# Kernel optimization log

Measured on AMD Instinct MI355X. Metric: run time of the kernel, lower is better.

## Reference

```python
import jax, jax.numpy as jnp
import numpy as np

P = 8  # patch size
EPS = 1e-5

def ln_ch(x, w, b):
    # WithBias LayerNorm over channel dim of (B,C,H,W): torch code flattens to (B,HW,C) and norms last dim
    mu = x.mean(axis=1, keepdims=True)
    var = ((x - mu) ** 2).mean(axis=1, keepdims=True)
    return (x - mu) / jnp.sqrt(var + EPS) * w[None, :, None, None] + b[None, :, None, None]

def conv1x1(x, w):
    # w: [C_out, C_in]
    return jnp.einsum('bchw,oc->bohw', x, w)

def dwconv3x3(x, w):
    # depthwise 3x3, w: [C,1,3,3]
    return jax.lax.conv_general_dilated(x, w, (1, 1), 'SAME', dimension_numbers=('NCHW', 'OIHW', 'NCHW'), feature_group_count=x.shape[1])

def patchify(x):
    b, c, H, W = x.shape
    return x.reshape(b, c, H // P, P, W // P, P).transpose(0, 1, 2, 4, 3, 5)  # b c h w p1 p2

def unpatchify(x):
    b, c, h, w, p1, p2 = x.shape
    return x.transpose(0, 1, 2, 4, 3, 5).reshape(b, c, h * p1, w * p2)

def setup_inputs() -> dict:
    key = jax.random.key(0)
    ks = jax.random.split(key, 16)
    B, C, H, W = 4, 64, 256, 256
    hid = 2 * C  # ffn_expansion_factor=2
    s = 0.02
    return {
        'x': jax.random.normal(ks[0], (B, C, H, W), jnp.float32),
        'evt': jax.random.normal(ks[1], (B, C, H, W), jnp.float32),
        'ln1i_w': jnp.ones((C,), jnp.float32), 'ln1i_b': jnp.zeros((C,), jnp.float32),
        'ln1e_w': jnp.ones((C,), jnp.float32), 'ln1e_b': jnp.zeros((C,), jnp.float32),
        'w_q': jax.random.normal(ks[2], (2 * C, C), jnp.float32) * s,
        'dw_q': jax.random.normal(ks[3], (2 * C, 1, 3, 3), jnp.float32) * s,
        'w_kv': jax.random.normal(ks[4], (4 * C, C), jnp.float32) * s,
        'dw_kv': jax.random.normal(ks[5], (4 * C, 1, 3, 3), jnp.float32) * s,
        'lnA_w': jnp.ones((2 * C,), jnp.float32), 'lnA_b': jnp.zeros((2 * C,), jnp.float32),
        'w_po_attn': jax.random.normal(ks[6], (C, 2 * C), jnp.float32) * s,
        'ln2_w': jnp.ones((C,), jnp.float32), 'ln2_b': jnp.zeros((C,), jnp.float32),
        'w_pi': jax.random.normal(ks[7], (2 * hid, C), jnp.float32) * s,
        'fft_param': jnp.ones((2 * hid, 1, 1, P, P // 2 + 1), jnp.float32),
        'dw_ffn': jax.random.normal(ks[8], (2 * hid, 1, 3, 3), jnp.float32) * s,
        'w_po_ffn': jax.random.normal(ks[9], (C, hid), jnp.float32) * s,
    }

def reference(x, evt, ln1i_w, ln1i_b, ln1e_w, ln1e_b, w_q, dw_q, w_kv, dw_kv, lnA_w, lnA_b, w_po_attn, ln2_w, ln2_b, w_pi, fft_param, dw_ffn, w_po_ffn):
    # ---- EventFSAS cross attention ----
    xn = ln_ch(x, ln1i_w, ln1i_b)
    en = ln_ch(evt, ln1e_w, ln1e_b)
    q = dwconv3x3(conv1x1(xn, w_q), dw_q)               # (B,2C,H,W)
    kv = dwconv3x3(conv1x1(en, w_kv), dw_kv)            # (B,4C,H,W)
    k, v = jnp.split(kv, 2, axis=1)
    qf = jnp.fft.rfft2(patchify(q))                      # (B,2C,h,w,8,5) complex
    kf = jnp.fft.rfft2(patchify(k))
    out = jnp.fft.irfft2(qf * kf, s=(P, P))
    out = ln_ch(unpatchify(out), lnA_w, lnA_b)
    x = x + conv1x1(v * out, w_po_attn)
    # ---- DFFN ----
    y = conv1x1(ln_ch(x, ln2_w, ln2_b), w_pi)            # (B,4C,H,W)
    yf = jnp.fft.rfft2(patchify(y)) * fft_param
    y = unpatchify(jnp.fft.irfft2(yf, s=(P, P)))
    y = dwconv3x3(y, dw_ffn)
    y1, y2 = jnp.split(y, 2, axis=1)
    y = jax.nn.gelu(y1, approximate=False) * y2          # torch nn.GELU is exact erf form
    return x + conv1x1(y, w_po_ffn)
```

## Files before the change

### kernel.cpp

```cpp
#include <hip/hip_runtime.h>

#define HW 65536
#define NPOS 262144

typedef unsigned int   u32;
typedef unsigned short u16;
typedef __attribute__((ext_vector_type(8))) short v8s;
typedef __attribute__((ext_vector_type(4))) float f32x4;
typedef __attribute__((ext_vector_type(2))) float f32x2;

__device__ __forceinline__ float bf2f(u16 h){
  union { u32 u; float f; } c; c.u = ((u32)h) << 16; return c.f;
}
__device__ __forceinline__ u16 f2bf(float f){
  union { u32 u; float f; } c; c.f = f;
  u32 r = c.u + 0x7fffu + ((c.u >> 16) & 1u);
  return (u16)(r >> 16);
}
__device__ __forceinline__ u32 pk2(float a, float b){
  return (u32)f2bf(a) | ((u32)f2bf(b) << 16);
}
__device__ __forceinline__ v8s as8(uint4 u){
  union { uint4 a; v8s b; } c; c.a = u; return c.b;
}
__device__ __forceinline__ f32x2 up2(u32 u){
  union { u32 u; float f; } lo, hi;
  lo.u = u << 16; hi.u = u & 0xffff0000u;
  f32x2 r; r.x = lo.f; r.y = hi.f; return r;
}
__device__ __forceinline__ float gelu_exact(float x){
  return 0.5f*x*(1.0f+erff(x*0.70710678118654752f));
}

__device__ void fold_w(const float* __restrict__ W, int rows,
                       const float* __restrict__ lw, const float* __restrict__ lb,
                       u16* __restrict__ Wf, float* __restrict__ A, float* __restrict__ B){
  int tid = threadIdx.x;
  for (int e = tid; e < rows*64; e += 256) Wf[e] = f2bf(lw[e & 63] * W[e]);
  for (int r = tid; r < rows; r += 256){
    float a = 0.f, b2 = 0.f;
    for (int c = 0; c < 64; c++){ float w = W[r*64+c]; a += lw[c]*w; b2 += lb[c]*w; }
    A[r] = a; B[r] = b2;
  }
}

__global__ void k_prep(const float* __restrict__ M, float* __restrict__ g,
    const float* wq,  const float* l1iw, const float* l1ib, u16* wqf,  float* aq,  float* bq,
    const float* wkv, const float* l1ew, const float* l1eb, u16* wkvf, float* akv, float* bkv,
    const float* wpi, const float* l2w,  const float* l2b,  u16* wpif, float* api, float* bpi,
    const float* wpa, u16* wpaf, const float* wpf, u16* wpff)
{
  int blk = blockIdx.x, tid = threadIdx.x;
  if (blk < 64){
    int t = blk*256 + tid;
    int c = t >> 6, uv = t & 63, u = uv >> 3, v = uv & 7;
    const float* mc = M + c*40;
    const float ctab[8] = {1.f, 0.70710678118654752f, 0.f, -0.70710678118654752f,
                           -1.f, -0.70710678118654752f, 0.f, 0.70710678118654752f};
    float acc = 0.f;
    for (int k1=0;k1<8;k1++)
      for (int k2=0;k2<8;k2++){
        float s = (k2<=4) ? mc[k1*5+k2] : mc[(((8-k1)&7)*5) + (8-k2)];
        acc += s * ctab[(k1*u + k2*v)&7];
      }
    g[t] = acc * (1.f/64.f);
  } else if (blk == 64){ fold_w(wq, 128, l1iw, l1ib, wqf, aq, bq); }
  else if (blk == 65){ fold_w(wkv, 256, l1ew, l1eb, wkvf, akv, bkv); }
  else if (blk == 66){ fold_w(wpi, 256, l2w, l2b, wpif, api, bpi); }
  else if (blk == 67){ for (int e=tid; e<64*128; e+=256) wpaf[e] = f2bf(wpa[e]); }
  else               { for (int e=tid; e<64*128; e+=256) wpff[e] = f2bf(wpf[e]); }
}

__global__ void k_prep2(const float* __restrict__ g, u16* __restrict__ CM){
  int c = blockIdx.x;
  const float* gc = g + (size_t)c*64;
  u16* cm = CM + (size_t)c*4096;
  for (int e = threadIdx.x; e < 4096; e += 256){
    int o = e >> 6, i = e & 63;
    int du = ((o>>3) - (i>>3)) & 7, dv = ((o&7) - (i&7)) & 7;
    cm[e] = f2bf(gc[du*8 + dv]);
  }
}

struct GA {
  const float* src; const u16* Wf; const float* Af; const float* Bf;
  u32* dst; int o0; int dstOffP; int Cdp; int b0; int pxbase;
};

template<int NZ>
__global__ __launch_bounds__(256) void k_gemm64(GA a0, GA a1){
  GA a = (blockIdx.y == 0) ? a0 : a1;
  __shared__ uint4 lsX[128*8];
  __shared__ uint4 lsW[64*NZ*8];
  __shared__ float2 sPart[256];
  __shared__ float2 sStat[128];
  int tid = threadIdx.x;
  int px = tid & 127, hf = tid >> 7;
  int p0 = a.pxbase + blockIdx.x*128;
  int b = p0 >> 16, hwb = p0 & 65535;
  {
    const uint4* wsrc = (const uint4*)(a.Wf + (size_t)a.o0*64);
    #pragma unroll
    for (int i=0; i<NZ*2; i++){
      int idx = i*256 + tid, row = idx>>3, s = idx&7;
      lsW[row*8 + (s ^ (row&7))] = wsrc[idx];
    }
  }
  {
    const float* sp = a.src + (size_t)b*64*HW + hwb + px + (size_t)(hf*32)*HW;
    float e[32];
    #pragma unroll
    for (int c=0;c<32;c++) e[c] = sp[(size_t)c*HW];
    float sm = 0.f, sq = 0.f;
    #pragma unroll
    for (int c=0;c<32;c++){ sm += e[c]; sq += e[c]*e[c]; }
    uint4* xrow = lsX + px*8;
    #pragma unroll
    for (int sl=0; sl<4; sl++){
      uint4 pkv;
      pkv.x = pk2(e[sl*8+0], e[sl*8+1]); pkv.y = pk2(e[sl*8+2], e[sl*8+3]);
      pkv.z = pk2(e[sl*8+4], e[sl*8+5]); pkv.w = pk2(e[sl*8+6], e[sl*8+7]);
      xrow[(hf*4+sl) ^ (px&7)] = pkv;
    }
    sPart[tid] = make_float2(sm, sq);
  }
  __syncthreads();
  if (tid < 128){
    float2 A = sPart[tid], B = sPart[tid+128];
    float s = A.x + B.x, q = A.y + B.y;
    float mu = s*(1.f/64.f);
    float var = q*(1.f/64.f) - mu*mu;
    sStat[tid] = make_float2(mu, rsqrtf(fmaxf(var,0.f)+1e-5f));
  }
  __syncthreads();
  int w = tid>>6, l = tid&63, g = l>>4, c15 = l&15;
  float2 stv[2];
  #pragma unroll
  for (int pp=0;pp<2;pp++) stv[pp] = sStat[w*32 + pp*16 + c15];

  #pragma unroll
  for (int z=0; z<NZ; z++){
    f32x4 acc[2][4];
    #pragma unroll
    for (int pp=0;pp<2;pp++)
      #pragma unroll
      for (int po=0;po<4;po++) acc[pp][po] = (f32x4){0.f,0.f,0.f,0.f};
    #pragma unroll
    for (int kk=0; kk<2; kk++){
      v8s wf[4], xf[2];
      #pragma unroll
      for (int po=0;po<4;po++){ int row = z*64 + po*16 + c15; wf[po] = as8(lsW[row*8 + ((kk*4+g) ^ (row&7))]); }
      #pragma unroll
      for (int pp=0;pp<2;pp++){ int row = w*32 + pp*16 + c15; xf[pp] = as8(lsX[row*8 + ((kk*4+g) ^ (row&7))]); }
      #pragma unroll
      for (int pp=0;pp<2;pp++)
        #pragma unroll
        for (int po=0;po<4;po++)
          acc[pp][po] = __builtin_amdgcn_mfma_f32_16x16x32_bf16(wf[po], xf[pp], acc[pp][po], 0,0,0);
    }
    size_t obaseP = ((size_t)(b - a.b0)*a.Cdp + a.dstOffP + z*32)*HW + hwb + w*32;
    #pragma unroll
    for (int po=0;po<4;po++)
      #pragma unroll
      for (int j2=0;j2<2;j2++){
        int oc = po*16 + g*4 + j2*2;
        float A0 = a.Af[a.o0 + z*64 + oc],   B0 = a.Bf[a.o0 + z*64 + oc];
        float A1 = a.Af[a.o0 + z*64 + oc+1], B1 = a.Bf[a.o0 + z*64 + oc+1];
        int ocp = po*8 + g*2 + j2;
        u32* dp = a.dst + obaseP + (size_t)ocp*HW + c15;
        #pragma unroll
        for (int pp=0;pp<2;pp++){
          float lo = stv[pp].y*(acc[pp][po][j2*2  ] - stv[pp].x*A0) + B0;
          float hi = stv[pp].y*(acc[pp][po][j2*2+1] - stv[pp].x*A1) + B1;
          dp[pp*16] = pk2(lo, hi);
        }
      }
  }
}

__global__ __launch_bounds__(256) void k_gemm_attn(
    const float* __restrict__ x, const u32* __restrict__ orawp, const u32* __restrict__ vbp,
    const float* __restrict__ lnw, const float* __restrict__ lnb,
    const u16* __restrict__ Wf, float* __restrict__ out)
{
  __shared__ uint4 lsX[128*16];
  __shared__ uint4 lsW[64*16];
  __shared__ float2 sPart[256];
  __shared__ float2 sStat[128];
  int tid = threadIdx.x;
  int p0 = blockIdx.x*128;
  int b = p0 >> 16, hwb = p0 & 65535;
  int px = tid & 127, hf = tid >> 7;
  {
    const uint4* wsrc = (const uint4*)Wf;
    #pragma unroll
    for (int i=0;i<4;i++){
      int idx = i*256 + tid, row = idx>>4, s = idx&15;
      lsW[row*16 + (s ^ (row&15))] = wsrc[idx];
    }
  }
  const u32* orp = orawp + ((size_t)b*64 + hf*32)*HW + hwb + px;
  {
    u32 r32[32];
    #pragma unroll
    for (int i=0;i<32;i++) r32[i] = orp[(size_t)i*HW];
    float sum = 0.f, ssq = 0.f;
    #pragma unroll
    for (int sl=0; sl<8; sl++){
      u32 wds[4];
      #pragma unroll
      for (int q2=0;q2<4;q2++){
        u32 wv = r32[sl*4+q2];
        float fl = bf2f((u16)(wv&0xffff)), fh = bf2f((u16)(wv>>16));
        sum += fl + fh; ssq += fl*fl + fh*fh;
        wds[q2] = wv;
      }
      int s = hf*8 + sl;
      lsX[px*16 + (s ^ (px&15))] = make_uint4(wds[0],wds[1],wds[2],wds[3]);
    }
    sPart[tid] = make_float2(sum, ssq);
  }
  __syncthreads();
  if (tid < 128){
    float2 A = sPart[tid], B = sPart[tid+128];
    float s = A.x + B.x, q = A.y + B.y;
    float mu = s*(1.f/128.f);
    float var = q*(1.f/128.f) - mu*mu;
    sStat[tid] = make_float2(mu, rsqrtf(fmaxf(var,0.f)+1e-5f));
  }
  __syncthreads();
  {
    float2 st = sStat[px];
    const u32* vp = vbp + ((size_t)b*64 + hf*32)*HW + hwb + px;
    u32 v32[32];
    #pragma unroll
    for (int i=0;i<32;i++) v32[i] = vp[(size_t)i*HW];
    #pragma unroll
    for (int sl=0; sl<8; sl++){
      int s = hf*8 + sl;
      int li = px*16 + (s ^ (px&15));
      uint4 raw = lsX[li];
      u32 wds[4] = {raw.x, raw.y, raw.z, raw.w};
      u32 ow[4];
      #pragma unroll
      for (int q2=0;q2<4;q2++){
        int ch = hf*64 + sl*8 + q2*2;
        float e0 = bf2f((u16)(wds[q2]&0xffff)), e1 = bf2f((u16)(wds[q2]>>16));
        u32 vv = v32[sl*4+q2];
        float v0 = bf2f((u16)(vv&0xffff)), v1 = bf2f((u16)(vv>>16));
        float r0 = ((e0-st.x)*st.y*lnw[ch  ] + lnb[ch  ])*v0;
        float r1 = ((e1-st.x)*st.y*lnw[ch+1] + lnb[ch+1])*v1;
        ow[q2] = pk2(r0, r1);
      }
      lsX[li] = make_uint4(ow[0],ow[1],ow[2],ow[3]);
    }
  }
  __syncthreads();
  int w4 = tid>>6, l = tid&63, g = l>>4, c15 = l&15;
  f32x4 acc[2][4];
  #pragma unroll
  for (int pp=0;pp<2;pp++)
    #pragma unroll
    for (int po=0;po<4;po++) acc[pp][po] = (f32x4){0.f,0.f,0.f,0.f};
  #pragma unroll
  for (int kk=0; kk<4; kk++){
    v8s wf[4], xf[2];
    #pragma unroll
    for (int po=0;po<4;po++){ int row = po*16 + c15; wf[po] = as8(lsW[row*16 + ((kk*4+g) ^ (row&15))]); }
    #pragma unroll
    for (int pp=0;pp<2;pp++){ int row = w4*32 + pp*16 + c15; xf[pp] = as8(lsX[row*16 + ((kk*4+g) ^ (row&15))]); }
    #pragma unroll
    for (int pp=0;pp<2;pp++)
      #pragma unroll
      for (int po=0;po<4;po++)
        acc[pp][po] = __builtin_amdgcn_mfma_f32_16x16x32_bf16(wf[po], xf[pp], acc[pp][po], 0,0,0);
  }
  size_t obase = (size_t)b*64*HW + hwb + w4*32;
  #pragma unroll
  for (int po=0;po<4;po++)
    #pragma unroll
    for (int j=0;j<4;j++){
      int oc = po*16 + g*4 + j;
      const float* xs = x + obase + (size_t)oc*HW + c15;
      float* dp = out + obase + (size_t)oc*HW + c15;
      #pragma unroll
      for (int pp=0;pp<2;pp++) dp[pp*16] = xs[pp*16] + acc[pp][po][j];
    }
}

__global__ __launch_bounds__(256) void k_gemm_ffn(
    const u32* __restrict__ y3gp, const u16* __restrict__ Wf, float* __restrict__ out,
    int pxbase, int b0)
{
  __shared__ uint4 lsX[128*16];
  __shared__ uint4 lsW[64*16];
  int tid = threadIdx.x;
  int p0 = pxbase + blockIdx.x*128;
  int b = p0 >> 16, hwb = p0 & 65535;
  int px = tid & 127, hf = tid >> 7;
  {
    const uint4* wsrc = (const uint4*)Wf;
    #pragma unroll
    for (int i=0;i<4;i++){
      int idx = i*256 + tid, row = idx>>4, s = idx&15;
      lsW[row*16 + (s ^ (row&15))] = wsrc[idx];
    }
  }
  const u32* yp = y3gp + ((size_t)(b-b0)*64 + hf*32)*HW + hwb + px;
  {
    u32 r32[32];
    #pragma unroll
    for (int i=0;i<32;i++) r32[i] = yp[(size_t)i*HW];
    #pragma unroll
    for (int sl=0; sl<8; sl++){
      int s = hf*8 + sl;
      lsX[px*16 + (s ^ (px&15))] = make_uint4(r32[sl*4+0],r32[sl*4+1],r32[sl*4+2],r32[sl*4+3]);
    }
  }
  __syncthreads();
  int w4 = tid>>6, l = tid&63, g = l>>4, c15 = l&15;
  f32x4 acc[2][4];
  #pragma unroll
  for (int pp=0;pp<2;pp++)
    #pragma unroll
    for (int po=0;po<4;po++) acc[pp][po] = (f32x4){0.f,0.f,0.f,0.f};
  #pragma unroll
  for (int kk=0; kk<4; kk++){
    v8s wf[4], xf[2];
    #pragma unroll
    for (int po=0;po<4;po++){ int row = po*16 + c15; wf[po] = as8(lsW[row*16 + ((kk*4+g) ^ (row&15))]); }
    #pragma unroll
    for (int pp=0;pp<2;pp++){ int row = w4*32 + pp*16 + c15; xf[pp] = as8(lsX[row*16 + ((kk*4+g) ^ (row&15))]); }
    #pragma unroll
    for (int pp=0;pp<2;pp++)
      #pragma unroll
      for (int po=0;po<4;po++)
        acc[pp][po] = __builtin_amdgcn_mfma_f32_16x16x32_bf16(wf[po], xf[pp], acc[pp][po], 0,0,0);
  }
  size_t obase = (size_t)b*64*HW + hwb + w4*32;
  #pragma unroll
  for (int po=0;po<4;po++)
    #pragma unroll
    for (int j=0;j<4;j++){
      int oc = po*16 + g*4 + j;
      float* dp = out + obase + (size_t)oc*HW + c15;
      #pragma unroll
      for (int pp=0;pp<2;pp++) dp[pp*16] = dp[pp*16] + acc[pp][po][j];
    }
}

__device__ __forceinline__ void dw8p_acc2(const u32* __restrict__ sp,
    const float* __restrict__ w9lo, const float* __restrict__ w9hi,
    int h, int w8, f32x2 a2[8])
{
  #pragma unroll
  for (int r=0;r<3;r++){
    int hh = h + r - 1;
    if (hh < 0 || hh > 255) continue;
    const u32* rp = sp + hh*256 + w8;
    uint4 ua = *(const uint4*)rp;
    uint4 ub = *(const uint4*)(rp+4);
    u32 e[8] = {ua.x,ua.y,ua.z,ua.w,ub.x,ub.y,ub.z,ub.w};
    u32 lef = (w8 > 0)   ? rp[-1] : 0u;
    u32 rig = (w8 < 248) ? rp[8]  : 0u;
    f32x2 vm[10];
    vm[0] = up2(lef);
    #pragma unroll
    for (int j=0;j<8;j++) vm[j+1] = up2(e[j]);
    vm[9] = up2(rig);
    f32x2 wa = {w9lo[r*3  ], w9hi[r*3  ]};
    f32x2 wb = {w9lo[r*3+1], w9hi[r*3+1]};
    f32x2 wc = {w9lo[r*3+2], w9hi[r*3+2]};
    #pragma unroll
    for (int j=0;j<8;j++)
      a2[j] += vm[j]*wa + vm[j+1]*wb + vm[j+2]*wc;
  }
}

__global__ __launch_bounds__(256) void k_dw8p(
    const u32* __restrict__ src, const float* __restrict__ wgt, int c0,
    u32* __restrict__ dstp, int dstOffP, int prMask, int prShift, int srcStride, int srcBase)
{
  int t = blockIdx.x*256 + threadIdx.x;
  int w8 = (t & 31)*8, h = (t>>5) & 255;
  int plane = t >> 13;
  int pr = plane & prMask, b = plane >> prShift;
  const u32* sp = src + ((size_t)(b*srcStride + srcBase + pr))*HW;
  const float* w9 = wgt + (size_t)(c0 + 2*pr)*9;
  f32x2 a2[8];
  #pragma unroll
  for (int j=0;j<8;j++) a2[j] = (f32x2){0.f,0.f};
  dw8p_acc2(sp, w9, w9+9, h, w8, a2);
  u32* dp = dstp + ((size_t)(b*64 + dstOffP + pr))*HW + h*256 + w8;
  uint4 s0, s1;
  s0.x=pk2(a2[0].x,a2[0].y); s0.y=pk2(a2[1].x,a2[1].y); s0.z=pk2(a2[2].x,a2[2].y); s0.w=pk2(a2[3].x,a2[3].y);
  s1.x=pk2(a2[4].x,a2[4].y); s1.y=pk2(a2[5].x,a2[5].y); s1.z=pk2(a2[6].x,a2[6].y); s1.w=pk2(a2[7].x,a2[7].y);
  *(uint4*)dp = s0; *(uint4*)(dp+4) = s1;
}

__global__ __launch_bounds__(256) void k_dw8gp(
    const u32* __restrict__ Y0p, const float* __restrict__ wgt, u32* __restrict__ Y3gp)
{
  int t = blockIdx.x*256 + threadIdx.x;
  int w8 = (t & 31)*8, h = (t>>5) & 255;
  int pc = t >> 13;
  int pr = pc & 63, bl = pc >> 6;
  const u32* spA = Y0p + ((size_t)(bl*128 + pr))*HW;
  const u32* spG = Y0p + ((size_t)(bl*128 + 64 + pr))*HW;
  const float* w9a = wgt + (size_t)(2*pr)*9;
  const float* w9g = wgt + (size_t)(128 + 2*pr)*9;
  f32x2 aA[8], aG[8];
  #pragma unroll
  for (int j=0;j<8;j++){ aA[j] = (f32x2){0.f,0.f}; aG[j] = (f32x2){0.f,0.f}; }
  dw8p_acc2(spA, w9a, w9a+9, h, w8, aA);
  dw8p_acc2(spG, w9g, w9g+9, h, w8, aG);
  u32* dp = Y3gp + ((size_t)(bl*64 + pr))*HW + h*256 + w8;
  uint4 s0, s1;
  s0.x=pk2(gelu_exact(aA[0].x)*aG[0].x, gelu_exact(aA[0].y)*aG[0].y);
  s0.y=pk2(gelu_exact(aA[1].x)*aG[1].x, gelu_exact(aA[1].y)*aG[1].y);
  s0.z=pk2(gelu_exact(aA[2].x)*aG[2].x, gelu_exact(aA[2].y)*aG[2].y);
  s0.w=pk2(gelu_exact(aA[3].x)*aG[3].x, gelu_exact(aA[3].y)*aG[3].y);
  s1.x=pk2(gelu_exact(aA[4].x)*aG[4].x, gelu_exact(aA[4].y)*aG[4].y);
  s1.y=pk2(gelu_exact(aA[5].x)*aG[5].x, gelu_exact(aA[5].y)*aG[5].y);
  s1.z=pk2(gelu_exact(aA[6].x)*aG[6].x, gelu_exact(aA[6].y)*aG[6].y);
  s1.w=pk2(gelu_exact(aA[7].x)*aG[7].x, gelu_exact(aA[7].y)*aG[7].y);
  *(uint4*)dp = s0; *(uint4*)(dp+4) = s1;
}

__global__ __launch_bounds__(256) void k_circqk4(
    const u32* __restrict__ bq, const u32* __restrict__ bk,
    const float* __restrict__ dwq, const float* __restrict__ dwk, int c0,
    u32* __restrict__ orawp, int oprBase, int cpb)
{
  __shared__ f32x2 qd[8][288];
  __shared__ f32x2 kd[8][288];
  int tid = threadIdx.x;
  int p = tid & 31, i = tid >> 5;
  int pr = blockIdx.y, b = blockIdx.z;
  int h0 = blockIdx.x*8;
  const u32* qp = bq + ((size_t)(b*cpb+pr))*HW;
  const u32* kp = bk + ((size_t)(b*cpb+pr))*HW;
  const float* wq9 = dwq + (size_t)(c0 + 2*pr)*9;
  const float* wk9 = dwk + (size_t)(c0 + 2*pr)*9;
  {
    f32x2 a2[8];
    #pragma unroll
    for (int j=0;j<8;j++) a2[j] = (f32x2){0.f,0.f};
    dw8p_acc2(qp, wq9, wq9+9, h0+i, p*8, a2);
    #pragma unroll
    for (int j=0;j<8;j++) qd[i][p*9+j] = a2[j];
  }
  {
    f32x2 a2[8];
    #pragma unroll
    for (int j=0;j<8;j++) a2[j] = (f32x2){0.f,0.f};
    dw8p_acc2(kp, wk9, wk9+9, h0+i, p*8, a2);
    #pragma unroll
    for (int j=0;j<8;j++) kd[i][p*9+j] = a2[j];
  }
  __syncthreads();
  f32x2 o[8];
  #pragma unroll
  for (int j=0;j<8;j++) o[j] = (f32x2){0.f,0.f};
  #pragma unroll
  for (int u=0;u<8;u++){
    int ku = (i-u)&7;
    f32x2 qv[8], kr[8];
    #pragma unroll
    for (int v=0;v<8;v++) qv[v] = qd[u][p*9+v];
    #pragma unroll
    for (int e=0;e<8;e++) kr[e] = kd[ku][p*9+e];
    #pragma unroll
    for (int v=0;v<8;v++){
      f32x2 qq = qv[v];
      #pragma unroll
      for (int j=0;j<8;j++)
        o[j] += qq * kr[(j-v)&7];
    }
  }
  u32* op = orawp + ((size_t)(b*64 + oprBase + pr))*HW + (size_t)(h0+i)*256 + p*8;
  uint4 s0, s1;
  s0.x=pk2(o[0].x,o[0].y); s0.y=pk2(o[1].x,o[1].y); s0.z=pk2(o[2].x,o[2].y); s0.w=pk2(o[3].x,o[3].y);
  s1.x=pk2(o[4].x,o[4].y); s1.y=pk2(o[5].x,o[5].y); s1.z=pk2(o[6].x,o[6].y); s1.w=pk2(o[7].x,o[7].y);
  *(uint4*)op = s0; *(uint4*)(op+4) = s1;
}

__global__ __launch_bounds__(256) void k_circg_mfma(
    u32* __restrict__ y, const u16* __restrict__ CM)
{
  __shared__ uint4 lsA[2][64*8];
  __shared__ uint4 lsB[2][64*8];
  int tid = threadIdx.x;
  int pr = blockIdx.y, b = blockIdx.z;
  int h0 = blockIdx.x*16;
  u32* plane = y + ((size_t)(b*128+pr))*HW;
  {
    const uint4* cmsrc = (const uint4*)(CM + (size_t)(2*pr)*4096);
    #pragma unroll
    for (int t=0; t<4; t++){
      int idx = t*256 + tid;
      int ch = idx >> 9, e = idx & 511;
      int row = e >> 3, s = e & 7;
      lsA[ch][row*8 + (s ^ (row&7))] = cmsrc[ch*512 + e];
    }
  }
  {
    #pragma unroll
    for (int t=0; t<2; t++){
      int rr = t*256 + tid;
      int n = rr >> 3, i = rr & 7;
      const u32* rp = plane + (size_t)(h0 + (n>>5)*8 + i)*256 + (n&31)*8;
      uint4 ua = *(const uint4*)rp;
      uint4 ub = *(const uint4*)(rp+4);
      u32 e[8] = {ua.x,ua.y,ua.z,ua.w,ub.x,ub.y,ub.z,ub.w};
      uint4 L, H;
      L.x = (e[0]&0xffffu) | (e[1]<<16);
      L.y = (e[2]&0xffffu) | (e[3]<<16);
      L.z = (e[4]&0xffffu) | (e[5]<<16);
      L.w = (e[6]&0xffffu) | (e[7]<<16);
      H.x = (e[0]>>16) | (e[1]&0xffff0000u);
      H.y = (e[2]>>16) | (e[3]&0xffff0000u);
      H.z = (e[4]>>16) | (e[5]&0xffff0000u);
      H.w = (e[6]>>16) | (e[7]&0xffff0000u);
      lsB[0][n*8 + (i ^ (n&7))] = L;
      lsB[1][n*8 + (i ^ (n&7))] = H;
    }
  }
  __syncthreads();
  int w = tid>>6, l = tid&63, g = l>>4, c15 = l&15;
  f32x4 acc[2][4];
  #pragma unroll
  for (int ch=0;ch<2;ch++)
    #pragma unroll
    for (int po=0;po<4;po++) acc[ch][po] = (f32x4){0.f,0.f,0.f,0.f};
  #pragma unroll
  for (int kk=0; kk<2; kk++){
    v8s bfr[2];
    { int row = w*16 + c15;
      bfr[0] = as8(lsB[0][row*8 + ((kk*4+g) ^ (row&7))]);
      bfr[1] = as8(lsB[1][row*8 + ((kk*4+g) ^ (row&7))]); }
    #pragma unroll
    for (int po=0;po<4;po++){
      int row = po*16 + c15;
      v8s aL = as8(lsA[0][row*8 + ((kk*4+g) ^ (row&7))]);
      v8s aH = as8(lsA[1][row*8 + ((kk*4+g) ^ (row&7))]);
      acc[0][po] = __builtin_amdgcn_mfma_f32_16x16x32_bf16(aL, bfr[0], acc[0][po], 0,0,0);
      acc[1][po] = __builtin_amdgcn_mfma_f32_16x16x32_bf16(aH, bfr[1], acc[1][po], 0,0,0);
    }
  }
  int patch = w*16 + c15;
  u32* pbase = plane + (size_t)(h0 + (patch>>5)*8)*256 + (patch&31)*8;
  #pragma unroll
  for (int po=0;po<4;po++){
    int oh = po*2 + (g>>1), ow4 = 4*(g&1);
    uint4 sv;
    sv.x = pk2(acc[0][po][0], acc[1][po][0]);
    sv.y = pk2(acc[0][po][1], acc[1][po][1]);
    sv.z = pk2(acc[0][po][2], acc[1][po][2]);
    sv.w = pk2(acc[0][po][3], acc[1][po][3]);
    *(uint4*)(pbase + (size_t)oh*256 + ow4) = sv;
  }
}

extern "C" void kernel_launch(void* const* d_in, const int* in_sizes, int n_in,
                              void* d_out, int out_size, void* d_ws, size_t ws_size,
                              hipStream_t stream)
{
  const float* x       = (const float*)d_in[0];
  const float* evt     = (const float*)d_in[1];
  const float* ln1i_w  = (const float*)d_in[2];
  const float* ln1i_b  = (const float*)d_in[3];
  const float* ln1e_w  = (const float*)d_in[4];
  const float* ln1e_b  = (const float*)d_in[5];
  const float* w_q     = (const float*)d_in[6];
  const float* dw_q    = (const float*)d_in[7];
  const float* w_kv    = (const float*)d_in[8];
  const float* dw_kv   = (const float*)d_in[9];
  const float* lnA_w   = (const float*)d_in[10];
  const float* lnA_b   = (const float*)d_in[11];
  const float* w_po_at = (const float*)d_in[12];
  const float* ln2_w   = (const float*)d_in[13];
  const float* ln2_b   = (const float*)d_in[14];
  const float* w_pi    = (const float*)d_in[15];
  const float* fft_par = (const float*)d_in[16];
  const float* dw_ffn  = (const float*)d_in[17];
  const float* w_poffn = (const float*)d_in[18];
  float* out = (float*)d_out;

  char* ws = (char*)d_ws;
  const size_t MiB = 1048576ull;
  bool big = (ws_size >= 200*MiB);
  size_t smOff = big ? 192*MiB : 160*MiB;
  char* sm = ws + smOff;
  float* G    = (float*)(sm);
  u16* WQF    = (u16*)(sm + 65536);
  u16* WKVF   = (u16*)(sm + 81920);
  u16* WPIF   = (u16*)(sm + 114688);
  u16* WPAF   = (u16*)(sm + 147456);
  u16* WPFF   = (u16*)(sm + 163840);
  float* AQ   = (float*)(sm + 180224);
  float* BQ   = (float*)(sm + 180736);
  float* AKV  = (float*)(sm + 181248);
  float* BKV  = (float*)(sm + 182272);
  float* API  = (float*)(sm + 183296);
  float* BPI  = (float*)(sm + 184320);
  u16* CMAT   = (u16*)(sm + 1*MiB);

  dim3 blk256(256);

  k_prep<<<69, blk256, 0, stream>>>(fft_par, G,
      w_q, ln1i_w, ln1i_b, WQF, AQ, BQ,
      w_kv, ln1e_w, ln1e_b, WKVF, AKV, BKV,
      w_pi, ln2_w, ln2_b, WPIF, API, BPI,
      w_po_at, WPAF, w_poffn, WPFF);
  k_prep2<<<256, blk256, 0, stream>>>(G, CMAT);

  if (big){
    u32* QBUF  = (u32*)(ws);
    u32* KBUF  = (u32*)(ws + 64*MiB);
    u32* ORAWp = (u32*)(ws + 128*MiB);
    u32* PV    = (u32*)(ws + 64*MiB);
    u32* VBUFp = (u32*)(ws);
    u32* Y0p   = (u32*)(ws);
    u32* Y3Gp  = (u32*)(ws + 128*MiB);

    GA qa = {x,   WQF,  AQ,  BQ,  QBUF, 0, 0, 64, 0, 0};
    GA ka = {evt, WKVF, AKV, BKV, KBUF, 0, 0, 64, 0, 0};
    k_gemm64<2><<<dim3(2048,2,1), blk256, 0, stream>>>(qa, ka);
    k_circqk4<<<dim3(32,64,4), blk256, 0, stream>>>(QBUF, KBUF, dw_q, dw_kv, 0, ORAWp, 0, 64);
    GA va = {evt, WKVF, AKV, BKV, PV, 128, 0, 64, 0, 0};
    k_gemm64<2><<<dim3(2048,1,1), blk256, 0, stream>>>(va, va);
    k_dw8p<<<8192, blk256, 0, stream>>>(PV, dw_kv, 128, VBUFp, 0, 63, 6, 64, 0);
    k_gemm_attn<<<2048, blk256, 0, stream>>>(x, ORAWp, VBUFp, lnA_w, lnA_b, WPAF, out);
    GA pa = {out, WPIF, API, BPI, Y0p, 0, 0, 128, 0, 0};
    k_gemm64<4><<<dim3(2048,1,1), blk256, 0, stream>>>(pa, pa);
    k_circg_mfma<<<dim3(16,128,4), blk256, 0, stream>>>(Y0p, CMAT);
    k_dw8gp<<<8192, blk256, 0, stream>>>(Y0p, dw_ffn, Y3Gp);
    k_gemm_ffn<<<2048, blk256, 0, stream>>>(Y3Gp, WPFF, out, 0, 0);
  } else {
    u32* P1p   = (u32*)(ws);
    u32* ORAWp = (u32*)(ws + 32*MiB);
    u32* P2p   = (u32*)(ws + 96*MiB);
    u32* VBUFp = (u32*)(ws + 96*MiB);
    u32* Y0p   = (u32*)(ws);
    u32* Y3Gp  = (u32*)(ws + 64*MiB);

    for (int i=0;i<2;i++){
      GA qa = {x,   WQF,  AQ,  BQ,  P1p, 64*i, 0, 32, 0, 0};
      GA ka = {evt, WKVF, AKV, BKV, P2p, 64*i, 0, 32, 0, 0};
      k_gemm64<1><<<dim3(2048,2,1), blk256, 0, stream>>>(qa, ka);
      k_circqk4<<<dim3(32,32,4), blk256, 0, stream>>>(P1p, P2p, dw_q, dw_kv, 64*i, ORAWp, 32*i, 32);
    }
    for (int i=0;i<2;i++){
      GA va = {evt, WKVF, AKV, BKV, P1p, 128+64*i, 0, 32, 0, 0};
      k_gemm64<1><<<dim3(2048,1,1), blk256, 0, stream>>>(va, va);
      k_dw8p<<<4096, blk256, 0, stream>>>(P1p, dw_kv, 128+64*i, VBUFp, 32*i, 31, 5, 32, 0);
    }
    k_gemm_attn<<<2048, blk256, 0, stream>>>(x, ORAWp, VBUFp, lnA_w, lnA_b, WPAF, out);
    for (int h=0;h<2;h++){
      GA pa = {out, WPIF, API, BPI, Y0p, 0, 0, 128, 2*h, h*131072};
      k_gemm64<4><<<dim3(1024,1,1), blk256, 0, stream>>>(pa, pa);
      k_circg_mfma<<<dim3(16,128,2), blk256, 0, stream>>>(Y0p, CMAT);
      k_dw8gp<<<4096, blk256, 0, stream>>>(Y0p, dw_ffn, Y3Gp);
      k_gemm_ffn<<<1024, blk256, 0, stream>>>(Y3Gp, WPFF, out, h*131072, 2*h);
    }
  }
}
```

Before: 464.2 us.

## Compute patch circular correlation via row-wise 8-point real FFT in circqk kernel

Each thread now applies an 8-point real DFT to its 8-wide row of q and k after the depthwise conv. The column-direction circular convolution then becomes pointwise complex products per frequency bin instead of a full 8x8 direct convolution in the width direction, followed by an inverse real DFT before storing. This replaces 64 multiply-adds per column step with about 8 complex-product terms, cutting arithmetic in the inner loop. The cost is extra FFT/IFFT butterfly work and slightly different floating-point rounding.

Measured after the change: 449.8 us, median of 2. -3.1%, faster.

```diff
diff --git a/kernel.cpp b/kernel.cpp
--- a/kernel.cpp
+++ b/kernel.cpp
@@ -377,6 +377,22 @@
   }
 }
 
+__device__ __forceinline__ void rfft8(const f32x2 x[8], f32x2 F[8]){
+  f32x2 E0 = x[0]+x[2]+x[4]+x[6];
+  f32x2 E2 = x[0]-x[2]+x[4]-x[6];
+  f32x2 E1r = x[0]-x[4], E1i = x[6]-x[2];
+  f32x2 O0 = x[1]+x[3]+x[5]+x[7];
+  f32x2 O2 = x[1]-x[3]+x[5]-x[7];
+  f32x2 O1r = x[1]-x[5], O1i = x[7]-x[3];
+  const float C = 0.70710678118654752f;
+  f32x2 s = (O1r+O1i)*C, d = (O1i-O1r)*C;
+  F[0] = E0+O0;
+  F[1] = E1r+s;  F[2] = E1i+d;
+  F[3] = E2;     F[4] = -O2;
+  F[5] = E1r-s;  F[6] = d-E1i;
+  F[7] = E0-O0;
+}
+
 __global__ __launch_bounds__(256) void k_dw8p(
     const u32* __restrict__ src, const float* __restrict__ wgt, int c0,
     u32* __restrict__ dstp, int dstOffP, int prMask, int prShift, int srcStride, int srcBase)
@@ -443,41 +459,53 @@
   const float* wq9 = dwq + (size_t)(c0 + 2*pr)*9;
   const float* wk9 = dwk + (size_t)(c0 + 2*pr)*9;
   {
-    f32x2 a2[8];
+    f32x2 a2[8], F[8];
     #pragma unroll
     for (int j=0;j<8;j++) a2[j] = (f32x2){0.f,0.f};
     dw8p_acc2(qp, wq9, wq9+9, h0+i, p*8, a2);
-    #pragma unroll
-    for (int j=0;j<8;j++) qd[i][p*9+j] = a2[j];
-  }
-  {
-    f32x2 a2[8];
+    rfft8(a2, F);
+    #pragma unroll
+    for (int j=0;j<8;j++) qd[i][p*9+j] = F[j];
+  }
+  {
+    f32x2 a2[8], F[8];
     #pragma unroll
     for (int j=0;j<8;j++) a2[j] = (f32x2){0.f,0.f};
     dw8p_acc2(kp, wk9, wk9+9, h0+i, p*8, a2);
-    #pragma unroll
-    for (int j=0;j<8;j++) kd[i][p*9+j] = a2[j];
-  }
-  __syncthreads();
-  f32x2 o[8];
-  #pragma unroll
-  for (int j=0;j<8;j++) o[j] = (f32x2){0.f,0.f};
+    rfft8(a2, F);
+    #pragma unroll
+    for (int j=0;j<8;j++) kd[i][p*9+j] = F[j];
+  }
+  __syncthreads();
+  f32x2 A[8];
+  #pragma unroll
+  for (int j=0;j<8;j++) A[j] = (f32x2){0.f,0.f};
   #pragma unroll
   for (int u=0;u<8;u++){
     int ku = (i-u)&7;
-    f32x2 qv[8], kr[8];
-    #pragma unroll
-    for (int v=0;v<8;v++) qv[v] = qd[u][p*9+v];
-    #pragma unroll
-    for (int e=0;e<8;e++) kr[e] = kd[ku][p*9+e];
-    #pragma unroll
-    for (int v=0;v<8;v++){
-      f32x2 qq = qv[v];
-      #pragma unroll
-      for (int j=0;j<8;j++)
-        o[j] += qq * kr[(j-v)&7];
-    }
-  }
+    const f32x2* Q = &qd[u][p*9];
+    const f32x2* K = &kd[ku][p*9];
+    f32x2 q0=Q[0],q1=Q[1],q2=Q[2],q3=Q[3],q4=Q[4],q5=Q[5],q6=Q[6],q7=Q[7];
+    f32x2 k0=K[0],k1=K[1],k2=K[2],k3=K[3],k4=K[4],k5=K[5],k6=K[6],k7=K[7];
+    A[0] += q0*k0;
+    A[1] += q1*k1 - q2*k2;  A[2] += q1*k2 + q2*k1;
+    A[3] += q3*k3 - q4*k4;  A[4] += q3*k4 + q4*k3;
+    A[5] += q5*k5 - q6*k6;  A[6] += q5*k6 + q6*k5;
+    A[7] += q7*k7;
+  }
+  const float C = 0.70710678118654752f;
+  const float IV = 0.125f;
+  f32x2 a0=A[0], b4=A[7], r1=A[1], i1=A[2], r2=A[3], i2=A[4], r3=A[5], i3=A[6];
+  f32x2 t0 = a0+b4, t1 = a0-b4;
+  f32x2 o[8];
+  o[0] = (t0 + (r1+r2+r3)*2.f)*IV;
+  o[1] = (t1 + ((r1-i1)*C - i2 - (r3+i3)*C)*2.f)*IV;
+  o[2] = (t0 + (i3-i1-r2)*2.f)*IV;
+  o[3] = (t1 + (i2 - (r1+i1)*C + (r3-i3)*C)*2.f)*IV;
+  o[4] = (t0 + (r2-r1-r3)*2.f)*IV;
+  o[5] = (t1 + ((i1-r1)*C - i2 + (r3+i3)*C)*2.f)*IV;
+  o[6] = (t0 + (i1-r2-i3)*2.f)*IV;
+  o[7] = (t1 + ((r1+i1)*C + i2 + (i3-r3)*C)*2.f)*IV;
   u32* op = orawp + ((size_t)(b*64 + oprBase + pr))*HW + (size_t)(h0+i)*256 + p*8;
   uint4 s0, s1;
   s0.x=pk2(o[0].x,o[0].y); s0.y=pk2(o[1].x,o[1].y); s0.z=pk2(o[2].x,o[2].y); s0.w=pk2(o[3].x,o[3].y);
```
